# Performance work log

Measured on AMD Instinct MI355X. Metric: run time of the kernel, lower is better.

## Reference

```python
import jax, jax.numpy as jnp
import numpy as np

T, B, DIM, N_STATE = 2048, 16, 1024, 1024
EPS = 1e-6


def setup_inputs() -> dict:
    key = jax.random.key(0)
    kx, kk, kv, kq = jax.random.split(key, 4)
    xavier = np.sqrt(2.0 / (N_STATE + DIM)).astype(np.float32)
    return {
        "x": jax.random.normal(kx, (T, B, DIM), dtype=jnp.float32),
        "W_k": jax.random.normal(kk, (N_STATE, DIM), dtype=jnp.float32) * xavier,
        "W_v": jax.random.normal(kv, (N_STATE, DIM), dtype=jnp.float32) * xavier,
        "W_q": jax.random.normal(kq, (N_STATE, DIM), dtype=jnp.float32) * xavier,
    }


def reference(x, W_k, W_v, W_q):
    # Projections for all timesteps at once: [T, B, n]
    k = jnp.einsum("tbd,nd->tbn", x, W_k)
    v = jnp.einsum("tbd,nd->tbn", x, W_v)
    q = jnp.einsum("tbd,nd->tbn", x, W_q)
    # L2-normalize k per (t, b) over the state dim (matches k_t.norm(dim=-1))
    k_norm = k / (jnp.linalg.norm(k, axis=-1, keepdims=True) + EPS)

    Tn, Bn, n = k.shape
    S0 = jnp.zeros((Bn, n), dtype=x.dtype)

    def step(S, inp):
        k_t, v_t, q_t = inp
        # Delta update with OUTPUT gating + tanh nonlinearity
        S_new = jnp.tanh(S * (1.0 - k_t * k_t) + v_t * k_t)
        Sq = S_new * q_t
        out = Sq * jax.nn.silu(Sq)
        return S_new, out

    S_final, output = jax.lax.scan(step, S0, (k_norm, v, q))
    return output, S_final
```

## Files before the change

kernel.cpp:

```cpp
#include <hip/hip_runtime.h>
#include <hip/hip_fp16.h>

#define T_STEPS 2048
#define BATCH 16
#define DIMD 1024
#define NSTATE 1024
#define MROWS (T_STEPS * BATCH)
#define NCH (BATCH * NSTATE)

typedef _Float16 f16x8 __attribute__((ext_vector_type(8)));
typedef float f32x4 __attribute__((ext_vector_type(4)));

#define GAS(p) ((const __attribute__((address_space(1))) void*)(p))
#define LAS(p) ((__attribute__((address_space(3))) void*)(p))

__global__ void cvt_kernel(const float* __restrict__ src, _Float16* __restrict__ dst, int n8) {
  int i = blockIdx.x * blockDim.x + threadIdx.x;
  if (i >= n8) return;
  const float4* s4 = (const float4*)src;
  float4 a = s4[(size_t)i * 2];
  float4 b = s4[(size_t)i * 2 + 1];
  f16x8 o;
  o[0] = (_Float16)a.x; o[1] = (_Float16)a.y; o[2] = (_Float16)a.z; o[3] = (_Float16)a.w;
  o[4] = (_Float16)b.x; o[5] = (_Float16)b.y; o[6] = (_Float16)b.z; o[7] = (_Float16)b.w;
  *((f16x8*)dst + i) = o;
}

__global__ void cvtW_kernel(const float* __restrict__ wk, const float* __restrict__ wv,
                            const float* __restrict__ wq, _Float16* __restrict__ dst) {
  const float* src = blockIdx.y == 0 ? wk : blockIdx.y == 1 ? wv : wq;
  int i = blockIdx.x * blockDim.x + threadIdx.x;
  const float4* s4 = (const float4*)src;
  float4 a = s4[(size_t)i * 2];
  float4 b = s4[(size_t)i * 2 + 1];
  f16x8 o;
  o[0] = (_Float16)a.x; o[1] = (_Float16)a.y; o[2] = (_Float16)a.z; o[3] = (_Float16)a.w;
  o[4] = (_Float16)b.x; o[5] = (_Float16)b.y; o[6] = (_Float16)b.z; o[7] = (_Float16)b.w;
  *((f16x8*)dst + (size_t)blockIdx.y * (NSTATE * DIMD / 8) + i) = o;
}

__global__ __launch_bounds__(512, 1) void gemm_kernel(const _Float16* __restrict__ A,
                                                      const _Float16* __restrict__ Wcat,
                                                      _Float16* __restrict__ KVQt,
                                                      float* __restrict__ rnpart) {
  __shared__ _Float16 lds[65536];
  const int tid = threadIdx.x;
  const int lane = tid & 63;
  const int w = tid >> 6;
  const int wm = w >> 2;
  const int wn = w & 3;

  const int bid = blockIdx.x;
  const int swz = (bid & 7) * 192 + (bid >> 3);
  const int mat = swz >> 9;
  const int rem = swz & 511;
  const int tileM = rem >> 2;
  const int tileN = rem & 3;

  const _Float16* Ag = A + (size_t)tileM * 256 * DIMD;
  const _Float16* Bg = Wcat + (size_t)mat * NSTATE * DIMD + (size_t)tileN * 256 * DIMD;

  const int s0 = tid, s1 = tid + 512;
  const int sr0 = s0 >> 2, sc0 = ((s0 & 3) ^ ((s0 >> 3) & 3)) * 8;
  const int sr1 = s1 >> 2, sc1 = ((s1 & 3) ^ ((s1 >> 3) & 3)) * 8;

#define STAGE_H(G, buf, reg, TT, h)                                                     \
  do {                                                                                  \
    __builtin_amdgcn_global_load_lds(                                                   \
        GAS(G + (size_t)sr0 * DIMD + (TT) * 64 + (h) * 32 + sc0),                       \
        LAS(lds + (buf) * 32768 + (reg) * 8192 + s0 * 8), 16, 0, 0);                    \
    __builtin_amdgcn_global_load_lds(                                                   \
        GAS(G + (size_t)sr1 * DIMD + (TT) * 64 + (h) * 32 + sc1),                       \
        LAS(lds + (buf) * 32768 + (reg) * 8192 + s1 * 8), 16, 0, 0);                    \
  } while (0)

  f32x4 acc[8][4];
#pragma unroll
  for (int m = 0; m < 8; ++m)
#pragma unroll
    for (int n = 0; n < 4; ++n)
      acc[m][n] = (f32x4){0.f, 0.f, 0.f, 0.f};

  STAGE_H(Ag, 0, 0, 0, 0);
  STAGE_H(Bg, 0, 2, 0, 0);
  STAGE_H(Ag, 0, 1, 0, 1);
  STAGE_H(Bg, 0, 3, 0, 1);

  const int fr = lane & 15;
  const int cbp = ((lane >> 4) ^ ((fr >> 1) & 3)) * 8;

#define LDA(dst, region, mi)                                                            \
  dst = *(const f16x8*)(lds + buf * 32768 + (region) * 8192 +                           \
                        (wm * 128 + (mi) * 16 + fr) * 32 + cbp)
#define LDB(dst, region, ni)                                                            \
  dst = *(const f16x8*)(lds + buf * 32768 + (region) * 8192 +                           \
                        (wn * 64 + (ni) * 16 + fr) * 32 + cbp)

#define KTILE(T)                                                                        \
  do {                                                                                  \
    const int buf = (T) & 1, bufn = buf ^ 1;                                            \
    f16x8 aF[4], bF[4];                                                                 \
      \
    asm volatile("s_waitcnt vmcnt(4)" ::: "memory");                                    \
    __builtin_amdgcn_s_barrier();                                                       \
    __builtin_amdgcn_sched_barrier(0);                                                  \
    if ((T) < 15) STAGE_H(Ag, bufn, 0, (T) + 1, 0);                                     \
    _Pragma("unroll") for (int m = 0; m < 4; ++m) LDA(aF[m], 0, m);                     \
    _Pragma("unroll") for (int n = 0; n < 4; ++n) LDB(bF[n], 2, n);                     \
    asm volatile("s_waitcnt lgkmcnt(0)" ::: "memory");                                  \
    __builtin_amdgcn_sched_barrier(0);                                                  \
    __builtin_amdgcn_s_setprio(1);                                                      \
    _Pragma("unroll") for (int m = 0; m < 4; ++m) _Pragma("unroll") for (int n = 0; n < 4; ++n) \
        acc[m][n] = __builtin_amdgcn_mfma_f32_16x16x32_f16(aF[m], bF[n], acc[m][n], 0, 0, 0); \
    __builtin_amdgcn_s_setprio(0);                                                      \
    __builtin_amdgcn_s_barrier();                                                       \
                 \
    if ((T) < 15) STAGE_H(Bg, bufn, 2, (T) + 1, 0);                                     \
    _Pragma("unroll") for (int m = 0; m < 4; ++m) LDA(aF[m], 0, m + 4);                 \
    asm volatile("s_waitcnt lgkmcnt(0)" ::: "memory");                                  \
    __builtin_amdgcn_sched_barrier(0);                                                  \
    __builtin_amdgcn_s_setprio(1);                                                      \
    _Pragma("unroll") for (int m = 0; m < 4; ++m) _Pragma("unroll") for (int n = 0; n < 4; ++n) \
        acc[m + 4][n] = __builtin_amdgcn_mfma_f32_16x16x32_f16(aF[m], bF[n], acc[m + 4][n], 0, 0, 0); \
    __builtin_amdgcn_s_setprio(0);                                                      \
    __builtin_amdgcn_s_barrier();                                                       \
      \
    if ((T) < 15) {                                                                     \
      asm volatile("s_waitcnt vmcnt(4)" ::: "memory");                                  \
    } else {                                                                            \
      asm volatile("s_waitcnt vmcnt(0)" ::: "memory");                                  \
    }                                                                                   \
    __builtin_amdgcn_s_barrier();                                                       \
    __builtin_amdgcn_sched_barrier(0);                                                  \
    if ((T) < 15) STAGE_H(Ag, bufn, 1, (T) + 1, 1);                                     \
    _Pragma("unroll") for (int m = 0; m < 4; ++m) LDA(aF[m], 1, m);                     \
    _Pragma("unroll") for (int n = 0; n < 4; ++n) LDB(bF[n], 3, n);                     \
    asm volatile("s_waitcnt lgkmcnt(0)" ::: "memory");                                  \
    __builtin_amdgcn_sched_barrier(0);                                                  \
    __builtin_amdgcn_s_setprio(1);                                                      \
    _Pragma("unroll") for (int m = 0; m < 4; ++m) _Pragma("unroll") for (int n = 0; n < 4; ++n) \
        acc[m][n] = __builtin_amdgcn_mfma_f32_16x16x32_f16(aF[m], bF[n], acc[m][n], 0, 0, 0); \
    __builtin_amdgcn_s_setprio(0);                                                      \
    __builtin_amdgcn_s_barrier();                                                       \
                 \
    if ((T) < 15) STAGE_H(Bg, bufn, 3, (T) + 1, 1);                                     \
    _Pragma("unroll") for (int m = 0; m < 4; ++m) LDA(aF[m], 1, m + 4);                 \
    asm volatile("s_waitcnt lgkmcnt(0)" ::: "memory");                                  \
    __builtin_amdgcn_sched_barrier(0);                                                  \
    __builtin_amdgcn_s_setprio(1);                                                      \
    _Pragma("unroll") for (int m = 0; m < 4; ++m) _Pragma("unroll") for (int n = 0; n < 4; ++n) \
        acc[m + 4][n] = __builtin_amdgcn_mfma_f32_16x16x32_f16(aF[m], bF[n], acc[m + 4][n], 0, 0, 0); \
    __builtin_amdgcn_s_setprio(0);                                                      \
    __builtin_amdgcn_s_barrier();                                                       \
  } while (0)

  KTILE(0);  KTILE(1);  KTILE(2);  KTILE(3);
  KTILE(4);  KTILE(5);  KTILE(6);  KTILE(7);
  KTILE(8);  KTILE(9);  KTILE(10); KTILE(11);
  KTILE(12); KTILE(13); KTILE(14); KTILE(15);

  const int cc = lane & 15;
  const int l4 = lane >> 4;
  _Float16* Cb = KVQt + (size_t)mat * ((size_t)MROWS * NSTATE) +
                 (size_t)(tileM * 2 + wm) * ((size_t)NCH * 8);
#pragma unroll
  for (int n = 0; n < 4; ++n)
#pragma unroll
    for (int j = 0; j < 4; ++j) {
      f16x8 pk;
#pragma unroll
      for (int m = 0; m < 8; ++m) pk[m] = (_Float16)acc[m][n][j];
      const int b = l4 * 4 + j;
      const int gcol = tileN * 256 + wn * 64 + n * 16 + cc;
      *(f16x8*)(Cb + ((size_t)(b * 1024 + gcol)) * 8) = pk;
    }

  if (mat == 0) {
#pragma unroll
    for (int m = 0; m < 8; ++m)
#pragma unroll
      for (int j = 0; j < 4; ++j) {
        float p = 0.f;
#pragma unroll
        for (int n = 0; n < 4; ++n) p += acc[m][n][j] * acc[m][n][j];
        p += __shfl_xor(p, 1);
        p += __shfl_xor(p, 2);
        p += __shfl_xor(p, 4);
        p += __shfl_xor(p, 8);
        if (cc == 0) {
          const int gr = tileM * 256 + wm * 128 + m * 16 + l4 * 4 + j;
          rnpart[(size_t)(tileN * 4 + wn) * MROWS + gr] = p;
        }
      }
  }
}

__global__ void rnfin_kernel(const float* __restrict__ part, float* __restrict__ rnT) {
  const int r = blockIdx.x * 256 + threadIdx.x;
  float s = 0.f;
#pragma unroll
  for (int i = 0; i < 16; ++i) s += part[(size_t)i * MROWS + r];
  rnT[(r & 15) * T_STEPS + (r >> 4)] = 1.f / (sqrtf(s) + 1e-6f);
}

#define STILE 16

#define LOADT(P, t0in)                                                        \
  do {                                                                        \
    const int tc = ((t0in) < T_STEPS) ? (t0in) : (T_STEPS - STILE);           \
    const size_t o0 = ((size_t)(tc >> 3) * NCH + c) * 8;                      \
    P##k0 = *(const f16x8*)(Kt + o0);                                         \
    P##k1 = *(const f16x8*)(Kt + o0 + (size_t)NCH * 8);                       \
    P##v0 = *(const f16x8*)(Vt + o0);                                         \
    P##v1 = *(const f16x8*)(Vt + o0 + (size_t)NCH * 8);                       \
    P##q0 = *(const f16x8*)(Qt + o0);                                         \
    P##q1 = *(const f16x8*)(Qt + o0 + (size_t)NCH * 8);                       \
    P##r0 = *(const f32x4*)(rnT + bb + tc);                                   \
    P##r1 = *(const f32x4*)(rnT + bb + tc + 4);                               \
    P##r2 = *(const f32x4*)(rnT + bb + tc + 8);                               \
    P##r3 = *(const f32x4*)(rnT + bb + tc + 12);                              \
  } while (0)

#define STEPT(P, t0)                                                          \
  do {                                                                        \
    float a2[STILE], b2[STILE], qf[STILE];                                    \
    _Pragma("unroll") for (int i = 0; i < STILE; ++i) {                       \
      float kf = (float)((i < 8) ? P##k0[i & 7] : P##k1[i & 7]);              \
      float vf = (float)((i < 8) ? P##v0[i & 7] : P##v1[i & 7]);              \
      float rv = (i < 4) ? P##r0[i & 3]                                       \
               : (i < 8) ? P##r1[i & 3]                                       \
               : (i < 12) ? P##r2[i & 3] : P##r3[i & 3];                      \
      float kn = kf * rv;                                                     \
      a2[i] = L2E2 - (L2E2 * kn) * kn;                                        \
      b2[i] = L2E2 * (vf * kn);                                               \
      qf[i] = (float)((i < 8) ? P##q0[i & 7] : P##q1[i & 7]);                 \
    }                                                                         \
    _Pragma("unroll") for (int i = 0; i < STILE; ++i) {                       \
      float u = fmaf(S, a2[i], b2[i]);                                        \
      float e = __builtin_amdgcn_exp2f(u);                                    \
      float r = __builtin_amdgcn_rcpf(e + 1.f);                               \
      S = fmaf(-2.f, r, 1.f);                                                 \
      float z = S * qf[i];                                                    \
      float sg = __builtin_amdgcn_rcpf(1.f + __builtin_amdgcn_exp2f(-L2E * z)); \
      out[(size_t)((t0) + i) * NCH + c] = z * z * sg;                         \
    }                                                                         \
  } while (0)

__global__ __launch_bounds__(64) void scan_kernel(const _Float16* __restrict__ Kt,
                                                  const _Float16* __restrict__ Vt,
                                                  const _Float16* __restrict__ Qt,
                                                  const float* __restrict__ rnT,
                                                  float* __restrict__ out,
                                                  float* __restrict__ sfin) {
  const int c = blockIdx.x * 64 + threadIdx.x;
  const int bb = (c >> 10) * T_STEPS;
  constexpr float L2E2 = 2.8853900817779268f;
  constexpr float L2E = 1.4426950408889634f;
  float S = 0.f;
  f16x8 Ak0, Ak1, Av0, Av1, Aq0, Aq1;
  f16x8 Bk0, Bk1, Bv0, Bv1, Bq0, Bq1;
  f16x8 Ck0, Ck1, Cv0, Cv1, Cq0, Cq1;
  f32x4 Ar0, Ar1, Ar2, Ar3, Br0, Br1, Br2, Br3, Cr0, Cr1, Cr2, Cr3;

  LOADT(A, 0);
  LOADT(B, STILE);
  for (int t0 = 0; t0 + 3 * STILE <= T_STEPS; t0 += 3 * STILE) {
    LOADT(C, t0 + 2 * STILE);
    STEPT(A, t0);
    LOADT(A, t0 + 3 * STILE);
    STEPT(B, t0 + STILE);
    LOADT(B, t0 + 4 * STILE);
    STEPT(C, t0 + 2 * STILE);
  }
  STEPT(A, T_STEPS - 2 * STILE);
  STEPT(B, T_STEPS - STILE);
  sfin[c] = S;
}

extern "C" void kernel_launch(void* const* d_in, const int* in_sizes, int n_in,
                              void* d_out, int out_size, void* d_ws, size_t ws_size,
                              hipStream_t stream) {
  const float* x = (const float*)d_in[0];
  const float* Wk = (const float*)d_in[1];
  const float* Wv = (const float*)d_in[2];
  const float* Wq = (const float*)d_in[3];

  char* ws = (char*)d_ws;
  _Float16* xh = (_Float16*)ws;
  _Float16* Wh = (_Float16*)(ws + 67108864ull);
  _Float16* KVQt = (_Float16*)(ws + 67108864ull + 6291456ull);
  float* rnpart = (float*)(ws + 67108864ull + 6291456ull + 201326592ull);
  float* rnT = (float*)(ws + 67108864ull + 6291456ull + 201326592ull + 2097152ull);

  int n8x = MROWS * DIMD / 8;
  cvt_kernel<<<(n8x + 255) / 256, 256, 0, stream>>>(x, xh, n8x);
  cvtW_kernel<<<dim3(NSTATE * DIMD / 8 / 256, 3), 256, 0, stream>>>(Wk, Wv, Wq, Wh);

  gemm_kernel<<<1536, 512, 0, stream>>>(xh, Wh, KVQt, rnpart);

  rnfin_kernel<<<MROWS / 256, 256, 0, stream>>>(rnpart, rnT);

  const _Float16* Kt = KVQt;
  const _Float16* Vt = KVQt + (size_t)MROWS * NSTATE;
  const _Float16* Qt = KVQt + 2ull * MROWS * NSTATE;
  float* outp = (float*)d_out;
  scan_kernel<<<NCH / 64, 64, 0, stream>>>(Kt, Vt, Qt, rnT, outp, outp + (size_t)MROWS * NSTATE);
}
```

Measured before the change: 381.8 us.

## Software-pipeline LDS fragment reads one phase ahead of MFMA blocks in GEMM

Restructures the projection GEMM's k-loop so the LDS fragment reads for the next MFMA phase are issued before the barrier that precedes it, and the first A/B fragments of the next k-tile are prefetched at the end of the current one. The aim is to hide LDS read latency behind barriers and global loads instead of stalling on lgkmcnt right before each MFMA batch. It changes the barrier and vmcnt placement, which raises the risk of LDS races and adds a prologue.

```diff
diff --git a/kernel.cpp b/kernel.cpp
--- a/kernel.cpp
+++ b/kernel.cpp
@@ -81,83 +81,101 @@
     for (int n = 0; n < 4; ++n)
       acc[m][n] = (f32x4){0.f, 0.f, 0.f, 0.f};
 
+  const int fr = lane & 15;
+  const int cbp = ((lane >> 4) ^ ((fr >> 1) & 3)) * 8;
+
+  f16x8 aF[4], bF[4];
+
+#define READS8(B, RA, RB)                                                               \
+  do {                                                                                  \
+    _Pragma("unroll") for (int m = 0; m < 4; ++m)                                       \
+        aF[m] = *(const f16x8*)(lds + (B) * 32768 + (RA) * 8192 +                       \
+                                (wm * 128 + m * 16 + fr) * 32 + cbp);                   \
+    _Pragma("unroll") for (int n = 0; n < 4; ++n)                                       \
+        bF[n] = *(const f16x8*)(lds + (B) * 32768 + (RB) * 8192 +                       \
+                                (wn * 64 + n * 16 + fr) * 32 + cbp);                    \
+  } while (0)
+
+#define READS4(B, RA)                                                                   \
+  do {                                                                                  \
+    _Pragma("unroll") for (int m = 0; m < 4; ++m)                                       \
+        aF[m] = *(const f16x8*)(lds + (B) * 32768 + (RA) * 8192 +                       \
+                                (wm * 128 + (m + 4) * 16 + fr) * 32 + cbp);             \
+  } while (0)
+
+#define MFMA_LO                                                                         \
+  _Pragma("unroll") for (int m = 0; m < 4; ++m)                                         \
+  _Pragma("unroll") for (int n = 0; n < 4; ++n)                                         \
+      acc[m][n] = __builtin_amdgcn_mfma_f32_16x16x32_f16(aF[m], bF[n], acc[m][n], 0, 0, 0)
+
+#define MFMA_HI                                                                         \
+  _Pragma("unroll") for (int m = 0; m < 4; ++m)                                         \
+  _Pragma("unroll") for (int n = 0; n < 4; ++n)                                         \
+      acc[m + 4][n] = __builtin_amdgcn_mfma_f32_16x16x32_f16(aF[m], bF[n], acc[m + 4][n], 0, 0, 0)
+
+#define LGKM0_SB                                                                        \
+  asm volatile("s_waitcnt lgkmcnt(0)" ::: "memory");                                    \
+  __builtin_amdgcn_sched_barrier(0)
+
+#define KT(T)                                                                           \
+  do {                                                                                  \
+    const int buf = (T) & 1, bufn = buf ^ 1;                                            \
+                                \
+    __builtin_amdgcn_s_barrier();                                                       \
+    LGKM0_SB;                                                                           \
+    __builtin_amdgcn_s_setprio(1); MFMA_LO; __builtin_amdgcn_s_setprio(0);              \
+    __builtin_amdgcn_s_barrier();                                                       \
+    READS4(buf, 0);                                                                     \
+    if ((T) <= 14) STAGE_H(Bg, bufn, 2, (T) + 1, 0);                                    \
+    __builtin_amdgcn_sched_barrier(0);                                                  \
+                                                      \
+    __builtin_amdgcn_s_barrier();                                                       \
+    LGKM0_SB;                                                                           \
+    __builtin_amdgcn_s_setprio(1); MFMA_HI; __builtin_amdgcn_s_setprio(0);              \
+    if ((T) <= 14) { asm volatile("s_waitcnt vmcnt(4)" ::: "memory"); }                 \
+    else           { asm volatile("s_waitcnt vmcnt(0)" ::: "memory"); }                 \
+    __builtin_amdgcn_s_barrier();                        \
+    __builtin_amdgcn_sched_barrier(0);                                                  \
+    READS8(buf, 1, 3);                                                                  \
+    if ((T) <= 14) STAGE_H(Ag, bufn, 1, (T) + 1, 1);                                    \
+    __builtin_amdgcn_sched_barrier(0);                                                  \
+                                                                \
+    __builtin_amdgcn_s_barrier();                                                       \
+    LGKM0_SB;                                                                           \
+    __builtin_amdgcn_s_setprio(1); MFMA_LO; __builtin_amdgcn_s_setprio(0);              \
+    __builtin_amdgcn_s_barrier();                                                       \
+    READS4(buf, 1);                                                                     \
+    if ((T) <= 14) STAGE_H(Bg, bufn, 3, (T) + 1, 1);                                    \
+    __builtin_amdgcn_sched_barrier(0);                                                  \
+                                                      \
+    __builtin_amdgcn_s_barrier();                                                       \
+    LGKM0_SB;                                                                           \
+    __builtin_amdgcn_s_setprio(1); MFMA_HI; __builtin_amdgcn_s_setprio(0);              \
+    if ((T) <= 14) {                                                                    \
+      asm volatile("s_waitcnt vmcnt(4)" ::: "memory");                                  \
+      __builtin_amdgcn_s_barrier();                  \
+      __builtin_amdgcn_sched_barrier(0);                                                \
+      READS8(bufn, 0, 2);                                                               \
+      if ((T) <= 13) STAGE_H(Ag, buf, 0, (T) + 2, 0);                                   \
+      __builtin_amdgcn_sched_barrier(0);                                                \
+    }                                                                                   \
+  } while (0)
+
   STAGE_H(Ag, 0, 0, 0, 0);
   STAGE_H(Bg, 0, 2, 0, 0);
   STAGE_H(Ag, 0, 1, 0, 1);
   STAGE_H(Bg, 0, 3, 0, 1);
-
-  const int fr = lane & 15;
-  const int cbp = ((lane >> 4) ^ ((fr >> 1) & 3)) * 8;
-
-#define LDA(dst, region, mi)                                                            \
-  dst = *(const f16x8*)(lds + buf * 32768 + (region) * 8192 +                           \
-                        (wm * 128 + (mi) * 16 + fr) * 32 + cbp)
-#define LDB(dst, region, ni)                                                            \
-  dst = *(const f16x8*)(lds + buf * 32768 + (region) * 8192 +                           \
-                        (wn * 64 + (ni) * 16 + fr) * 32 + cbp)
-
-#define KTILE(T)                                                                        \
-  do {                                                                                  \
-    const int buf = (T) & 1, bufn = buf ^ 1;                                            \
-    f16x8 aF[4], bF[4];                                                                 \
-      \
-    asm volatile("s_waitcnt vmcnt(4)" ::: "memory");                                    \
-    __builtin_amdgcn_s_barrier();                                                       \
-    __builtin_amdgcn_sched_barrier(0);                                                  \
-    if ((T) < 15) STAGE_H(Ag, bufn, 0, (T) + 1, 0);                                     \
-    _Pragma("unroll") for (int m = 0; m < 4; ++m) LDA(aF[m], 0, m);                     \
-    _Pragma("unroll") for (int n = 0; n < 4; ++n) LDB(bF[n], 2, n);                     \
-    asm volatile("s_waitcnt lgkmcnt(0)" ::: "memory");                                  \
-    __builtin_amdgcn_sched_barrier(0);                                                  \
-    __builtin_amdgcn_s_setprio(1);                                                      \
-    _Pragma("unroll") for (int m = 0; m < 4; ++m) _Pragma("unroll") for (int n = 0; n < 4; ++n) \
-        acc[m][n] = __builtin_amdgcn_mfma_f32_16x16x32_f16(aF[m], bF[n], acc[m][n], 0, 0, 0); \
-    __builtin_amdgcn_s_setprio(0);                                                      \
-    __builtin_amdgcn_s_barrier();                                                       \
-                 \
-    if ((T) < 15) STAGE_H(Bg, bufn, 2, (T) + 1, 0);                                     \
-    _Pragma("unroll") for (int m = 0; m < 4; ++m) LDA(aF[m], 0, m + 4);                 \
-    asm volatile("s_waitcnt lgkmcnt(0)" ::: "memory");                                  \
-    __builtin_amdgcn_sched_barrier(0);                                                  \
-    __builtin_amdgcn_s_setprio(1);                                                      \
-    _Pragma("unroll") for (int m = 0; m < 4; ++m) _Pragma("unroll") for (int n = 0; n < 4; ++n) \
-        acc[m + 4][n] = __builtin_amdgcn_mfma_f32_16x16x32_f16(aF[m], bF[n], acc[m + 4][n], 0, 0, 0); \
-    __builtin_amdgcn_s_setprio(0);                                                      \
-    __builtin_amdgcn_s_barrier();                                                       \
-      \
-    if ((T) < 15) {                                                                     \
-      asm volatile("s_waitcnt vmcnt(4)" ::: "memory");                                  \
-    } else {                                                                            \
-      asm volatile("s_waitcnt vmcnt(0)" ::: "memory");                                  \
-    }                                                                                   \
-    __builtin_amdgcn_s_barrier();                                                       \
-    __builtin_amdgcn_sched_barrier(0);                                                  \
-    if ((T) < 15) STAGE_H(Ag, bufn, 1, (T) + 1, 1);                                     \
-    _Pragma("unroll") for (int m = 0; m < 4; ++m) LDA(aF[m], 1, m);                     \
-    _Pragma("unroll") for (int n = 0; n < 4; ++n) LDB(bF[n], 3, n);                     \
-    asm volatile("s_waitcnt lgkmcnt(0)" ::: "memory");                                  \
-    __builtin_amdgcn_sched_barrier(0);                                                  \
-    __builtin_amdgcn_s_setprio(1);                                                      \
-    _Pragma("unroll") for (int m = 0; m < 4; ++m) _Pragma("unroll") for (int n = 0; n < 4; ++n) \
-        acc[m][n] = __builtin_amdgcn_mfma_f32_16x16x32_f16(aF[m], bF[n], acc[m][n], 0, 0, 0); \
-    __builtin_amdgcn_s_setprio(0);                                                      \
-    __builtin_amdgcn_s_barrier();                                                       \
-                 \
-    if ((T) < 15) STAGE_H(Bg, bufn, 3, (T) + 1, 1);                                     \
-    _Pragma("unroll") for (int m = 0; m < 4; ++m) LDA(aF[m], 1, m + 4);                 \
-    asm volatile("s_waitcnt lgkmcnt(0)" ::: "memory");                                  \
-    __builtin_amdgcn_sched_barrier(0);                                                  \
-    __builtin_amdgcn_s_setprio(1);                                                      \
-    _Pragma("unroll") for (int m = 0; m < 4; ++m) _Pragma("unroll") for (int n = 0; n < 4; ++n) \
-        acc[m + 4][n] = __builtin_amdgcn_mfma_f32_16x16x32_f16(aF[m], bF[n], acc[m + 4][n], 0, 0, 0); \
-    __builtin_amdgcn_s_setprio(0);                                                      \
-    __builtin_amdgcn_s_barrier();                                                       \
-  } while (0)
-
-  KTILE(0);  KTILE(1);  KTILE(2);  KTILE(3);
-  KTILE(4);  KTILE(5);  KTILE(6);  KTILE(7);
-  KTILE(8);  KTILE(9);  KTILE(10); KTILE(11);
-  KTILE(12); KTILE(13); KTILE(14); KTILE(15);
+  asm volatile("s_waitcnt vmcnt(4)" ::: "memory");
+  __builtin_amdgcn_s_barrier();
+  __builtin_amdgcn_sched_barrier(0);
+  READS8(0, 0, 2);
+  STAGE_H(Ag, 1, 0, 1, 0);
+  __builtin_amdgcn_sched_barrier(0);
+
+  KT(0);  KT(1);  KT(2);  KT(3);
+  KT(4);  KT(5);  KT(6);  KT(7);
+  KT(8);  KT(9);  KT(10); KT(11);
+  KT(12); KT(13); KT(14); KT(15);
 
   const int cc = lane & 15;
   const int l4 = lane >> 4;
```

Result: no change. 382.9 us (+0.3%).

## Split scan into a state-boundary pass and parallel chunked output pass

Applied to the files above, without the earlier changes.

The scan now runs in two passes. A first kernel runs the serial recurrence using only k, v and the norms, and saves the state every 128 steps. A second kernel launches 16 chunks per channel, 4096 blocks in total, each starting from its saved boundary state, and computes the outputs with the q gating and SiLU. This moves the store-heavy output work out of the serial critical path and gives it far more parallelism, at the cost of reading k and v twice and launching an extra kernel.

```diff
diff --git a/kernel.cpp b/kernel.cpp
--- a/kernel.cpp
+++ b/kernel.cpp
@@ -204,6 +204,75 @@
 }
 
 #define STILE 16
+constexpr float L2E2c = 2.8853900817779268f;
+constexpr float L2Ec = 1.4426950408889634f;
+
+#define LOADB(P, t0in)                                                        \
+  do {                                                                        \
+    const int tc = ((t0in) < T_STEPS) ? (t0in) : (T_STEPS - STILE);           \
+    const size_t o0 = ((size_t)(tc >> 3) * NCH + c) * 8;                      \
+    P##k0 = *(const f16x8*)(Kt + o0);                                         \
+    P##k1 = *(const f16x8*)(Kt + o0 + (size_t)NCH * 8);                       \
+    P##v0 = *(const f16x8*)(Vt + o0);                                         \
+    P##v1 = *(const f16x8*)(Vt + o0 + (size_t)NCH * 8);                       \
+    P##r0 = *(const f32x4*)(rnT + bb + tc);                                   \
+    P##r1 = *(const f32x4*)(rnT + bb + tc + 4);                               \
+    P##r2 = *(const f32x4*)(rnT + bb + tc + 8);                               \
+    P##r3 = *(const f32x4*)(rnT + bb + tc + 12);                              \
+  } while (0)
+
+#define STEPB(P, t0)                                                          \
+  do {                                                                        \
+    float a2[STILE], b2[STILE];                                               \
+    _Pragma("unroll") for (int i = 0; i < STILE; ++i) {                       \
+      float kf = (float)((i < 8) ? P##k0[i & 7] : P##k1[i & 7]);              \
+      float vf = (float)((i < 8) ? P##v0[i & 7] : P##v1[i & 7]);              \
+      float rv = (i < 4) ? P##r0[i & 3]                                       \
+               : (i < 8) ? P##r1[i & 3]                                       \
+               : (i < 12) ? P##r2[i & 3] : P##r3[i & 3];                      \
+      float kn = kf * rv;                                                     \
+      a2[i] = L2E2c - (L2E2c * kn) * kn;                                      \
+      b2[i] = L2E2c * (vf * kn);                                              \
+    }                                                                         \
+    _Pragma("unroll") for (int i = 0; i < STILE; ++i) {                       \
+      float u = fmaf(S, a2[i], b2[i]);                                        \
+      float e = __builtin_amdgcn_exp2f(u);                                    \
+      float r = __builtin_amdgcn_rcpf(e + 1.f);                               \
+      S = fmaf(-2.f, r, 1.f);                                                 \
+    }                                                                         \
+    if ((((t0) + STILE) & 127) == 0) {       \
+      const int j = ((t0) + STILE) >> 7;                                      \
+      if (j < 16) Sb[(size_t)(j - 1) * NCH + c] = S;                          \
+      else sfin[c] = S;                                                       \
+    }                                                                         \
+  } while (0)
+
+__global__ __launch_bounds__(64) void scan_bound_kernel(const _Float16* __restrict__ Kt,
+                                                        const _Float16* __restrict__ Vt,
+                                                        const float* __restrict__ rnT,
+                                                        float* __restrict__ Sb,
+                                                        float* __restrict__ sfin) {
+  const int c = blockIdx.x * 64 + threadIdx.x;
+  const int bb = (c >> 10) * T_STEPS;
+  float S = 0.f;
+  f16x8 Ak0, Ak1, Av0, Av1;
+  f16x8 Bk0, Bk1, Bv0, Bv1;
+  f16x8 Ck0, Ck1, Cv0, Cv1;
+  f32x4 Ar0, Ar1, Ar2, Ar3, Br0, Br1, Br2, Br3, Cr0, Cr1, Cr2, Cr3;
+
+  LOADB(A, 0);
+  LOADB(B, STILE);
+  for (int t0 = 0; t0 + 3 * STILE <= T_STEPS; t0 += 3 * STILE) {
+    LOADB(C, t0 + 2 * STILE);
+    STEPB(A, t0);
+    LOADB(A, t0 + 3 * STILE);
+    STEPB(B, t0 + STILE);
+    LOADB(B, t0 + 4 * STILE);
+    STEPB(C, t0 + 2 * STILE);
+  }
+  STEPB(A, T_STEPS - 2 * STILE);
+  STEPB(B, T_STEPS - STILE);
+}
 
 #define LOADT(P, t0in)                                                        \
   do {                                                                        \
@@ -231,8 +300,8 @@
                : (i < 8) ? P##r1[i & 3]                                       \
                : (i < 12) ? P##r2[i & 3] : P##r3[i & 3];                      \
       float kn = kf * rv;                                                     \
-      a2[i] = L2E2 - (L2E2 * kn) * kn;                                        \
-      b2[i] = L2E2 * (vf * kn);                                               \
+      a2[i] = L2E2c - (L2E2c * kn) * kn;                                      \
+      b2[i] = L2E2c * (vf * kn);                                              \
       qf[i] = (float)((i < 8) ? P##q0[i & 7] : P##q1[i & 7]);                 \
     }                                                                         \
     _Pragma("unroll") for (int i = 0; i < STILE; ++i) {                       \
@@ -241,40 +310,35 @@
       float r = __builtin_amdgcn_rcpf(e + 1.f);                               \
       S = fmaf(-2.f, r, 1.f);                                                 \
       float z = S * qf[i];                                                    \
-      float sg = __builtin_amdgcn_rcpf(1.f + __builtin_amdgcn_exp2f(-L2E * z)); \
+      float sg = __builtin_amdgcn_rcpf(1.f + __builtin_amdgcn_exp2f(-L2Ec * z)); \
       out[(size_t)((t0) + i) * NCH + c] = z * z * sg;                         \
     }                                                                         \
   } while (0)
 
-__global__ __launch_bounds__(64) void scan_kernel(const _Float16* __restrict__ Kt,
-                                                  const _Float16* __restrict__ Vt,
-                                                  const _Float16* __restrict__ Qt,
-                                                  const float* __restrict__ rnT,
-                                                  float* __restrict__ out,
-                                                  float* __restrict__ sfin) {
-  const int c = blockIdx.x * 64 + threadIdx.x;
+__global__ __launch_bounds__(64) void scan_chunk_kernel(const _Float16* __restrict__ Kt,
+                                                        const _Float16* __restrict__ Vt,
+                                                        const _Float16* __restrict__ Qt,
+                                                        const float* __restrict__ rnT,
+                                                        const float* __restrict__ Sb,
+                                                        float* __restrict__ out) {
+  const int chunk = blockIdx.x >> 8;
+  const int c = (blockIdx.x & 255) * 64 + threadIdx.x;
   const int bb = (c >> 10) * T_STEPS;
-  constexpr float L2E2 = 2.8853900817779268f;
-  constexpr float L2E = 1.4426950408889634f;
-  float S = 0.f;
+  float S = (chunk == 0) ? 0.f : Sb[(size_t)(chunk - 1) * NCH + c];
+  const int base = chunk * 128;
   f16x8 Ak0, Ak1, Av0, Av1, Aq0, Aq1;
   f16x8 Bk0, Bk1, Bv0, Bv1, Bq0, Bq1;
-  f16x8 Ck0, Ck1, Cv0, Cv1, Cq0, Cq1;
-  f32x4 Ar0, Ar1, Ar2, Ar3, Br0, Br1, Br2, Br3, Cr0, Cr1, Cr2, Cr3;
-
-  LOADT(A, 0);
-  LOADT(B, STILE);
-  for (int t0 = 0; t0 + 3 * STILE <= T_STEPS; t0 += 3 * STILE) {
-    LOADT(C, t0 + 2 * STILE);
-    STEPT(A, t0);
-    LOADT(A, t0 + 3 * STILE);
-    STEPT(B, t0 + STILE);
-    LOADT(B, t0 + 4 * STILE);
-    STEPT(C, t0 + 2 * STILE);
+  f32x4 Ar0, Ar1, Ar2, Ar3, Br0, Br1, Br2, Br3;
+
+  LOADT(A, base);
+#pragma unroll
+  for (int tt = 0; tt < 4; ++tt) {
+    const int t = base + tt * 32;
+    LOADT(B, t + STILE);
+    STEPT(A, t);
+    LOADT(A, t + 2 * STILE);
+    STEPT(B, t + STILE);
   }
-  STEPT(A, T_STEPS - 2 * STILE);
-  STEPT(B, T_STEPS - STILE);
-  sfin[c] = S;
 }
 
 extern "C" void kernel_launch(void* const* d_in, const int* in_sizes, int n_in,
@@ -291,6 +355,7 @@
   _Float16* KVQt = (_Float16*)(ws + 67108864ull + 6291456ull);
   float* rnpart = (float*)(ws + 67108864ull + 6291456ull + 201326592ull);
   float* rnT = (float*)(ws + 67108864ull + 6291456ull + 201326592ull + 2097152ull);
+  float* Sb = (float*)(ws + 67108864ull + 6291456ull + 201326592ull + 2097152ull + 131072ull);
 
   int n8x = MROWS * DIMD / 8;
   cvt_kernel<<<(n8x + 255) / 256, 256, 0, stream>>>(x, xh, n8x);
@@ -304,5 +369,8 @@
   const _Float16* Vt = KVQt + (size_t)MROWS * NSTATE;
   const _Float16* Qt = KVQt + 2ull * MROWS * NSTATE;
   float* outp = (float*)d_out;
-  scan_kernel<<<NCH / 64, 64, 0, stream>>>(Kt, Vt, Qt, rnT, outp, outp + (size_t)MROWS * NSTATE);
-}
+  float* sfin = outp + (size_t)MROWS * NSTATE;
+
+  scan_bound_kernel<<<NCH / 64, 64, 0, stream>>>(Kt, Vt, rnT, Sb, sfin);
+  scan_chunk_kernel<<<4096, 64, 0, stream>>>(Kt, Vt, Qt, rnT, Sb, outp);
+}
```

New measurement: 405.3 us. 6.2% more time.
